# Performance work log

Hardware: AMD Instinct MI355X
Metric: run time of the kernel (lower is better)

## Reference

```python
import jax, jax.numpy as jnp
import numpy as np

B, N, F_IN, H, C = 4, 2048, 128, 4, 32
NEG_SLOPE = 0.2
EDGE_DENSITY = 0.01  # ~20 avg degree


def setup_inputs() -> dict:
    key = jax.random.key(0)
    ks = jax.random.split(key, 6)
    x = jax.random.normal(ks[0], (B, N, F_IN), dtype=jnp.float32)
    adj = (jax.random.uniform(ks[1], (B, N, N)) < EDGE_DENSITY).astype(jnp.float32)
    # glorot-style scaled params
    W = jax.random.normal(ks[2], (F_IN, H * C), dtype=jnp.float32) * (2.0 / (F_IN + H * C)) ** 0.5
    att_src = jax.random.normal(ks[3], (H, C), dtype=jnp.float32) * (2.0 / (1 + C)) ** 0.5
    att_dst = jax.random.normal(ks[4], (H, C), dtype=jnp.float32) * (2.0 / (1 + C)) ** 0.5
    bias = jnp.zeros((H * C,), dtype=jnp.float32)
    return {"x": x, "adj": adj, "W": W, "att_src": att_src, "att_dst": att_dst, "bias": bias}


def reference(x, adj, W, att_src, att_dst, bias):
    b, n, _ = x.shape
    h, c = att_src.shape
    # add self-loops
    idx = jnp.arange(n)
    adj = adj.at[:, idx, idx].set(1.0)
    # linear projection: [B,N,H,C]
    out = (x @ W).reshape(b, n, h, c)
    a_src = jnp.einsum('bnhc,hc->bnh', out, att_src)
    a_dst = jnp.einsum('bnhc,hc->bnh', out, att_dst)
    # alpha[b,i,j,h] = a_src[b,i,h] + a_dst[b,j,h]  -> [B,N,N,H]
    alpha = a_src[:, :, None, :] + a_dst[:, None, :, :]
    alpha = jax.nn.leaky_relu(alpha, NEG_SLOPE)
    alpha = adj[..., None] * jnp.exp(alpha)
    # faithful to original: normalize over dim=1 (the i axis)
    alpha = alpha / alpha.sum(axis=1, keepdims=True)
    # out_i = sum_j alpha[b,i,j,h] * feat[b,j,h,c]
    o = jnp.einsum('bijh,bjhc->bihc', alpha, out)
    o = o.reshape(b, n, h * c) + bias
    return o
```

## Files before the change

kernel.cpp:

```cpp
#include <hip/hip_runtime.h>
#include <math.h>

#define BB 4
#define NN 2048
#define F_IN 128
#define HH 4
#define CC 32
#define HC 128
#define NEG_SLOPE 0.2f
#define CAP 96

__device__ __forceinline__ float lrelu(float v) {
    return v > 0.f ? v : NEG_SLOPE * v;
}

__global__ __launch_bounds__(256) void k_gemm(const float* __restrict__ x,
                                              const float* __restrict__ W,
                                              float* __restrict__ feat) {
    __shared__ float xs[32][F_IN];
    const long row0 = (long)blockIdx.x * 32;
    const int t = threadIdx.x;
    for (int idx = t; idx < 32 * F_IN; idx += 256)
        xs[idx >> 7][idx & 127] = x[row0 * F_IN + idx];
    __syncthreads();
    const int col = t & 127;
    const int rg  = t >> 7;
    float acc[16];
#pragma unroll
    for (int r = 0; r < 16; ++r) acc[r] = 0.f;
    for (int k = 0; k < F_IN; ++k) {
        float w = W[k * HC + col];
#pragma unroll
        for (int r = 0; r < 16; ++r)
            acc[r] += xs[rg + 2 * r][k] * w;
    }
#pragma unroll
    for (int r = 0; r < 16; ++r)
        feat[(row0 + rg + 2 * r) * HC + col] = acc[r];
}

__global__ void k_att(const float* __restrict__ feat,
                      const float* __restrict__ att_src,
                      const float* __restrict__ att_dst,
                      float* __restrict__ a_src,
                      float* __restrict__ a_dst,
                      float* __restrict__ denom) {
    int idx = blockIdx.x * blockDim.x + threadIdx.x;
    if (idx >= BB * NN * HH) return;
    int h = idx & 3;
    long bn = idx >> 2;
    const float* f = feat + bn * HC + h * CC;
    float s = 0.f, d = 0.f;
#pragma unroll
    for (int c = 0; c < CC; ++c) {
        float v = f[c];
        s += v * att_src[h * CC + c];
        d += v * att_dst[h * CC + c];
    }
    a_src[idx] = s;
    a_dst[idx] = d;
    denom[idx] = 0.f;
}

__global__ __launch_bounds__(256) void k_scan(const float4* __restrict__ adj4,
                                              const float* __restrict__ a_src,
                                              const float* __restrict__ a_dst,
                                              float* __restrict__ denom,
                                              int* __restrict__ cnt,
                                              unsigned short* __restrict__ nbr) {
    const int bi = blockIdx.x;
    const int b = bi >> 11;
    const int i = bi & (NN - 1);
    __shared__ int s_cnt;
    if (threadIdx.x == 0) s_cnt = 0;
    __syncthreads();
    const int t = threadIdx.x;
    const float4* row = adj4 + (long)bi * (NN / 4);
    float4 v0 = row[t];
    float4 v1 = row[t + 256];
    const float4 as4 = *(const float4*)(a_src + bi * 4);

#define PROC(val, jc)                                                          \
    if ((val) != 0.f || (jc) == i) {                                           \
        int slot = atomicAdd(&s_cnt, 1);                                       \
        if (slot < CAP) nbr[(long)bi * CAP + slot] = (unsigned short)(jc);     \
        const long jj = (((long)b << 11) + (jc)) * 4;                          \
        float4 ad = *(const float4*)(a_dst + jj);                              \
        atomicAdd(&denom[jj + 0], __expf(lrelu(as4.x + ad.x)));                \
        atomicAdd(&denom[jj + 1], __expf(lrelu(as4.y + ad.y)));                \
        atomicAdd(&denom[jj + 2], __expf(lrelu(as4.z + ad.z)));                \
        atomicAdd(&denom[jj + 3], __expf(lrelu(as4.w + ad.w)));                \
    }

    int j0 = 4 * t;
    PROC(v0.x, j0 + 0)
    PROC(v0.y, j0 + 1)
    PROC(v0.z, j0 + 2)
    PROC(v0.w, j0 + 3)
    int j1 = 4 * t + 1024;
    PROC(v1.x, j1 + 0)
    PROC(v1.y, j1 + 1)
    PROC(v1.z, j1 + 2)
    PROC(v1.w, j1 + 3)
#undef PROC

    __syncthreads();
    if (t == 0) cnt[bi] = min(s_cnt, CAP);
}

__global__ __launch_bounds__(128) void k_aggr(const float* __restrict__ feat,
                                              const float* __restrict__ a_src,
                                              const float* __restrict__ a_dst,
                                              const float* __restrict__ denom,
                                              const int* __restrict__ cnt,
                                              const unsigned short* __restrict__ nbr,
                                              const float* __restrict__ bias,
                                              float* __restrict__ out) {
    const int bi = blockIdx.x;
    const int b = bi >> 11;
    const int t = threadIdx.x;
    __shared__ float s_coef[CAP][HH];
    __shared__ int   s_j[CAP];
    const int n = cnt[bi];
    for (int s = t; s < n; s += 128)
        s_j[s] = nbr[(long)bi * CAP + s];
    __syncthreads();
    for (int idx = t; idx < n * HH; idx += 128) {
        int s = idx >> 2, h = idx & 3;
        long jj = (((long)b << 11) + s_j[s]) * 4 + h;
        float e = __expf(lrelu(a_src[bi * 4 + h] + a_dst[jj]));
        s_coef[s][h] = e / denom[jj];
    }
    __syncthreads();
    const int h = t >> 5;
    const float* fb = feat + ((long)b << 11) * HC + t;
    float a0 = 0.f, a1 = 0.f, a2 = 0.f, a3 = 0.f;
    int s = 0;
    for (; s + 4 <= n; s += 4) {
        int j0 = s_j[s + 0], j1 = s_j[s + 1], j2 = s_j[s + 2], j3 = s_j[s + 3];
        float c0 = s_coef[s + 0][h], c1 = s_coef[s + 1][h];
        float c2 = s_coef[s + 2][h], c3 = s_coef[s + 3][h];
        a0 += c0 * fb[(long)j0 * HC];
        a1 += c1 * fb[(long)j1 * HC];
        a2 += c2 * fb[(long)j2 * HC];
        a3 += c3 * fb[(long)j3 * HC];
    }
    for (; s < n; ++s)
        a0 += s_coef[s][h] * fb[(long)s_j[s] * HC];
    out[(long)bi * HC + t] = (a0 + a1) + (a2 + a3) + bias[t];
}

extern "C" void kernel_launch(void* const* d_in, const int* in_sizes, int n_in,
                              void* d_out, int out_size, void* d_ws, size_t ws_size,
                              hipStream_t stream) {
    const float* x       = (const float*)d_in[0];
    const float* adj     = (const float*)d_in[1];
    const float* W       = (const float*)d_in[2];
    const float* att_src = (const float*)d_in[3];
    const float* att_dst = (const float*)d_in[4];
    const float* bias    = (const float*)d_in[5];
    float* out = (float*)d_out;

    float* feat  = (float*)d_ws;
    float* a_src = feat  + (long)BB * NN * HC;
    float* a_dst = a_src + (long)BB * NN * HH;
    float* denom = a_dst + (long)BB * NN * HH;
    int*   cnt   = (int*)(denom + (long)BB * NN * HH);
    unsigned short* nbr = (unsigned short*)(cnt + (long)BB * NN);

    k_gemm<<<(BB * NN) / 32, 256, 0, stream>>>(x, W, feat);
    k_att<<<(BB * NN * HH + 255) / 256, 256, 0, stream>>>(feat, att_src, att_dst,
                                                          a_src, a_dst, denom);
    k_scan<<<BB * NN, 256, 0, stream>>>((const float4*)adj, a_src, a_dst, denom, cnt, nbr);
    k_aggr<<<BB * NN, 128, 0, stream>>>(feat, a_src, a_dst, denom, cnt, nbr, bias, out);
}
```

Measured before the change: 170.8 us.

## Tile adjacency scan and replace global denom atomics with per-tile partial sums

Fuses the attention-logit computation into the projection GEMM. The per-row adjacency scan becomes a 2D tiled scan with 256x128 tiles. Each tile builds a shared-memory edge list and accumulates column denominators in shared memory, writing one partial sum per row tile. A small kernel then reduces the partials into reciprocal denominators, so the global float atomics on denom disappear and the aggregation kernel multiplies by the reciprocal instead of dividing. Neighbour capacity drops from 96 to 64 and each tile's edge list is capped at 768. This risks truncation for unusually dense rows or tiles, and neighbour order becomes nondeterministic.

```diff
diff --git a/kernel.cpp b/kernel.cpp
--- a/kernel.cpp
+++ b/kernel.cpp
@@ -8,16 +8,27 @@
 #define CC 32
 #define HC 128
 #define NEG_SLOPE 0.2f
-#define CAP 96
+#define CAP 64
+#define RT 256
+#define CT 128
+#define NRT 8
+#define NCT 16
+#define LCAP 768
 
 __device__ __forceinline__ float lrelu(float v) {
     return v > 0.f ? v : NEG_SLOPE * v;
 }
 
-__global__ __launch_bounds__(256) void k_gemm(const float* __restrict__ x,
-                                              const float* __restrict__ W,
-                                              float* __restrict__ feat) {
+__global__ __launch_bounds__(256) void k_gemm_att(const float* __restrict__ x,
+                                                  const float* __restrict__ W,
+                                                  const float* __restrict__ att_src,
+                                                  const float* __restrict__ att_dst,
+                                                  float* __restrict__ feat,
+                                                  float* __restrict__ a_src,
+                                                  float* __restrict__ a_dst,
+                                                  int* __restrict__ cnt) {
     __shared__ float xs[32][F_IN];
+    __shared__ float fs[32][HC + 1];
     const long row0 = (long)blockIdx.x * 32;
     const int t = threadIdx.x;
     for (int idx = t; idx < 32 * F_IN; idx += 256)
@@ -35,118 +46,172 @@
             acc[r] += xs[rg + 2 * r][k] * w;
     }
 #pragma unroll
-    for (int r = 0; r < 16; ++r)
+    for (int r = 0; r < 16; ++r) {
         feat[(row0 + rg + 2 * r) * HC + col] = acc[r];
-}
-
-__global__ void k_att(const float* __restrict__ feat,
-                      const float* __restrict__ att_src,
-                      const float* __restrict__ att_dst,
-                      float* __restrict__ a_src,
-                      float* __restrict__ a_dst,
-                      float* __restrict__ denom) {
-    int idx = blockIdx.x * blockDim.x + threadIdx.x;
-    if (idx >= BB * NN * HH) return;
-    int h = idx & 3;
-    long bn = idx >> 2;
-    const float* f = feat + bn * HC + h * CC;
-    float s = 0.f, d = 0.f;
-#pragma unroll
-    for (int c = 0; c < CC; ++c) {
-        float v = f[c];
-        s += v * att_src[h * CC + c];
-        d += v * att_dst[h * CC + c];
-    }
-    a_src[idx] = s;
-    a_dst[idx] = d;
-    denom[idx] = 0.f;
-}
-
-__global__ __launch_bounds__(256) void k_scan(const float4* __restrict__ adj4,
-                                              const float* __restrict__ a_src,
-                                              const float* __restrict__ a_dst,
-                                              float* __restrict__ denom,
+        fs[rg + 2 * r][col] = acc[r];
+    }
+    __syncthreads();
+    if (t < 128) {
+        const int row = t & 31;
+        const int h   = t >> 5;
+        float s = 0.f, d = 0.f;
+#pragma unroll
+        for (int c = 0; c < CC; ++c) {
+            float v = fs[row][h * CC + c];
+            s += v * att_src[h * CC + c];
+            d += v * att_dst[h * CC + c];
+        }
+        a_src[(row0 + row) * 4 + h] = s;
+        a_dst[(row0 + row) * 4 + h] = d;
+    }
+    if (t < 32) cnt[blockIdx.x * 32 + t] = 0;
+}
+
+__global__ __launch_bounds__(256) void k_tile(const float4* __restrict__ adj4,
+                                              const float4* __restrict__ as4g,
+                                              const float4* __restrict__ ad4g,
                                               int* __restrict__ cnt,
-                                              unsigned short* __restrict__ nbr) {
-    const int bi = blockIdx.x;
-    const int b = bi >> 11;
-    const int i = bi & (NN - 1);
-    __shared__ int s_cnt;
-    if (threadIdx.x == 0) s_cnt = 0;
-    __syncthreads();
-    const int t = threadIdx.x;
-    const float4* row = adj4 + (long)bi * (NN / 4);
-    float4 v0 = row[t];
-    float4 v1 = row[t + 256];
-    const float4 as4 = *(const float4*)(a_src + bi * 4);
-
-#define PROC(val, jc)                                                          \
-    if ((val) != 0.f || (jc) == i) {                                           \
-        int slot = atomicAdd(&s_cnt, 1);                                       \
-        if (slot < CAP) nbr[(long)bi * CAP + slot] = (unsigned short)(jc);     \
-        const long jj = (((long)b << 11) + (jc)) * 4;                          \
-        float4 ad = *(const float4*)(a_dst + jj);                              \
-        atomicAdd(&denom[jj + 0], __expf(lrelu(as4.x + ad.x)));                \
-        atomicAdd(&denom[jj + 1], __expf(lrelu(as4.y + ad.y)));                \
-        atomicAdd(&denom[jj + 2], __expf(lrelu(as4.z + ad.z)));                \
-        atomicAdd(&denom[jj + 3], __expf(lrelu(as4.w + ad.w)));                \
-    }
-
-    int j0 = 4 * t;
-    PROC(v0.x, j0 + 0)
-    PROC(v0.y, j0 + 1)
-    PROC(v0.z, j0 + 2)
-    PROC(v0.w, j0 + 3)
-    int j1 = 4 * t + 1024;
-    PROC(v1.x, j1 + 0)
-    PROC(v1.y, j1 + 1)
-    PROC(v1.z, j1 + 2)
-    PROC(v1.w, j1 + 3)
-#undef PROC
-
-    __syncthreads();
-    if (t == 0) cnt[bi] = min(s_cnt, CAP);
+                                              unsigned short* __restrict__ nbr,
+                                              float4* __restrict__ partial) {
+    const int bx = blockIdx.x;
+    const int b  = bx >> 7;
+    const int rt = (bx >> 4) & 7;
+    const int ct = bx & 15;
+    const int i0 = rt * RT;
+    const int c0 = ct * CT;
+    const int t  = threadIdx.x;
+
+    __shared__ float4 as4[RT];
+    __shared__ float4 ad4[CT];
+    __shared__ float4 pd[CT];
+    __shared__ unsigned short blist[LCAP];
+    __shared__ int rowcnt[RT];
+    __shared__ int rowoff[RT];
+    __shared__ int nent;
+
+    as4[t] = as4g[(b << 11) + i0 + t];
+    if (t < CT) {
+        ad4[t] = ad4g[(b << 11) + c0 + t];
+        pd[t] = make_float4(0.f, 0.f, 0.f, 0.f);
+    }
+    rowcnt[t] = 0;
+    if (t == 0) nent = 0;
+    __syncthreads();
+
+    const float4* base = adj4 + ((long)((b << 11) + i0)) * (NN / 4) + (c0 >> 2);
+    int idx0 = t * 4;
+    float4 v = base[(idx0 >> 7) * (NN / 4) + ((idx0 & 127) >> 2)];
+    for (int s = 0; s < 32; ++s) {
+        const int idx = s * 1024 + t * 4;
+        const float4 cur = v;
+        if (s < 31) {
+            const int nx = idx + 1024;
+            v = base[(nx >> 7) * (NN / 4) + ((nx & 127) >> 2)];
+        }
+        const int il = idx >> 7;
+        const int j0 = idx & 127;
+        const int gi = i0 + il;
+#pragma unroll
+        for (int k = 0; k < 4; ++k) {
+            const float vv = (&cur.x)[k];
+            if (vv != 0.f || gi == c0 + j0 + k) {
+                int pos = atomicAdd(&nent, 1);
+                if (pos < LCAP) blist[pos] = (unsigned short)((il << 7) | (j0 + k));
+                atomicAdd(&rowcnt[il], 1);
+            }
+        }
+    }
+    __syncthreads();
+
+    {
+        int rc = rowcnt[t];
+        int bs = 0;
+        if (rc > 0) bs = atomicAdd(&cnt[(b << 11) + i0 + t], rc);
+        rowoff[t] = bs;
+    }
+    __syncthreads();
+
+    const int ne = min(nent, LCAP);
+    for (int e = t; e < ne; e += 256) {
+        const int pk = blist[e];
+        const int il = pk >> 7;
+        const int jl = pk & 127;
+        const float4 s4 = as4[il];
+        const float4 d4 = ad4[jl];
+        atomicAdd(&(&pd[jl].x)[0], __expf(lrelu(s4.x + d4.x)));
+        atomicAdd(&(&pd[jl].x)[1], __expf(lrelu(s4.y + d4.y)));
+        atomicAdd(&(&pd[jl].x)[2], __expf(lrelu(s4.z + d4.z)));
+        atomicAdd(&(&pd[jl].x)[3], __expf(lrelu(s4.w + d4.w)));
+        int slot = atomicAdd(&rowoff[il], 1);
+        if (slot < CAP)
+            nbr[((long)((b << 11) + i0 + il)) * CAP + slot] = (unsigned short)(c0 + jl);
+    }
+    __syncthreads();
+
+    if (t < CT)
+        partial[((long)(b * NRT + rt) << 11) + c0 + t] = pd[t];
+}
+
+__global__ __launch_bounds__(256) void k_rdenom(const float4* __restrict__ partial,
+                                                float4* __restrict__ rdenom) {
+    const int u = blockIdx.x * blockDim.x + threadIdx.x;
+    if (u >= BB * NN) return;
+    const int b = u >> 11;
+    const int j = u & 2047;
+    float4 s = make_float4(0.f, 0.f, 0.f, 0.f);
+#pragma unroll
+    for (int rt = 0; rt < NRT; ++rt) {
+        float4 p = partial[((long)(b * NRT + rt) << 11) + j];
+        s.x += p.x; s.y += p.y; s.z += p.z; s.w += p.w;
+    }
+    rdenom[u] = make_float4(1.f / s.x, 1.f / s.y, 1.f / s.z, 1.f / s.w);
 }
 
 __global__ __launch_bounds__(128) void k_aggr(const float* __restrict__ feat,
                                               const float* __restrict__ a_src,
-                                              const float* __restrict__ a_dst,
-                                              const float* __restrict__ denom,
+                                              const float4* __restrict__ ad4,
+                                              const float4* __restrict__ rd4,
                                               const int* __restrict__ cnt,
                                               const unsigned short* __restrict__ nbr,
                                               const float* __restrict__ bias,
                                               float* __restrict__ out) {
     const int bi = blockIdx.x;
-    const int b = bi >> 11;
-    const int t = threadIdx.x;
-    __shared__ float s_coef[CAP][HH];
-    __shared__ int   s_j[CAP];
-    const int n = cnt[bi];
-    for (int s = t; s < n; s += 128)
-        s_j[s] = nbr[(long)bi * CAP + s];
-    __syncthreads();
-    for (int idx = t; idx < n * HH; idx += 128) {
-        int s = idx >> 2, h = idx & 3;
-        long jj = (((long)b << 11) + s_j[s]) * 4 + h;
-        float e = __expf(lrelu(a_src[bi * 4 + h] + a_dst[jj]));
-        s_coef[s][h] = e / denom[jj];
+    const int b  = bi >> 11;
+    const int t  = threadIdx.x;
+    __shared__ float4 s_coef[CAP];
+    __shared__ int    s_j[CAP];
+    __shared__ float  s_as[4];
+    const int n = min(cnt[bi], CAP);
+    if (t < 4) s_as[t] = a_src[bi * 4 + t];
+    if (t < n) s_j[t] = nbr[(long)bi * CAP + t];
+    __syncthreads();
+    if (t < n) {
+        const int j = s_j[t];
+        const float4 ad = ad4[(b << 11) + j];
+        const float4 rd = rd4[(b << 11) + j];
+        float4 c;
+        c.x = __expf(lrelu(s_as[0] + ad.x)) * rd.x;
+        c.y = __expf(lrelu(s_as[1] + ad.y)) * rd.y;
+        c.z = __expf(lrelu(s_as[2] + ad.z)) * rd.z;
+        c.w = __expf(lrelu(s_as[3] + ad.w)) * rd.w;
+        s_coef[t] = c;
     }
     __syncthreads();
     const int h = t >> 5;
-    const float* fb = feat + ((long)b << 11) * HC + t;
+    const float* fb = feat + ((long)(b << 11)) * HC + t;
     float a0 = 0.f, a1 = 0.f, a2 = 0.f, a3 = 0.f;
     int s = 0;
     for (; s + 4 <= n; s += 4) {
         int j0 = s_j[s + 0], j1 = s_j[s + 1], j2 = s_j[s + 2], j3 = s_j[s + 3];
-        float c0 = s_coef[s + 0][h], c1 = s_coef[s + 1][h];
-        float c2 = s_coef[s + 2][h], c3 = s_coef[s + 3][h];
+        float c0 = (&s_coef[s + 0].x)[h], c1 = (&s_coef[s + 1].x)[h];
+        float c2 = (&s_coef[s + 2].x)[h], c3 = (&s_coef[s + 3].x)[h];
         a0 += c0 * fb[(long)j0 * HC];
         a1 += c1 * fb[(long)j1 * HC];
         a2 += c2 * fb[(long)j2 * HC];
         a3 += c3 * fb[(long)j3 * HC];
     }
     for (; s < n; ++s)
-        a0 += s_coef[s][h] * fb[(long)s_j[s] * HC];
+        a0 += (&s_coef[s].x)[h] * fb[(long)s_j[s] * HC];
     out[(long)bi * HC + t] = (a0 + a1) + (a2 + a3) + bias[t];
 }
 
@@ -161,16 +226,21 @@
     const float* bias    = (const float*)d_in[5];
     float* out = (float*)d_out;
 
-    float* feat  = (float*)d_ws;
-    float* a_src = feat  + (long)BB * NN * HC;
-    float* a_dst = a_src + (long)BB * NN * HH;
-    float* denom = a_dst + (long)BB * NN * HH;
-    int*   cnt   = (int*)(denom + (long)BB * NN * HH);
+    float* feat    = (float*)d_ws;
+    float* a_src   = feat    + (long)BB * NN * HC;
+    float* a_dst   = a_src   + (long)BB * NN * HH;
+    float* rdenom  = a_dst   + (long)BB * NN * HH;
+    float* partial = rdenom  + (long)BB * NN * HH;
+    int*   cnt     = (int*)(partial + (long)BB * NRT * NN * HH);
     unsigned short* nbr = (unsigned short*)(cnt + (long)BB * NN);
 
-    k_gemm<<<(BB * NN) / 32, 256, 0, stream>>>(x, W, feat);
-    k_att<<<(BB * NN * HH + 255) / 256, 256, 0, stream>>>(feat, att_src, att_dst,
-                                                          a_src, a_dst, denom);
-    k_scan<<<BB * NN, 256, 0, stream>>>((const float4*)adj, a_src, a_dst, denom, cnt, nbr);
-    k_aggr<<<BB * NN, 128, 0, stream>>>(feat, a_src, a_dst, denom, cnt, nbr, bias, out);
-}
+    k_gemm_att<<<(BB * NN) / 32, 256, 0, stream>>>(x, W, att_src, att_dst,
+                                                   feat, a_src, a_dst, cnt);
+    k_tile<<<BB * NRT * NCT, 256, 0, stream>>>((const float4*)adj, (const float4*)a_src,
+                                               (const float4*)a_dst, cnt, nbr,
+                                               (float4*)partial);
+    k_rdenom<<<(BB * NN + 255) / 256, 256, 0, stream>>>((const float4*)partial,
+                                                        (float4*)rdenom);
+    k_aggr<<<BB * NN, 128, 0, stream>>>(feat, a_src, (const float4*)a_dst,
+                                        (const float4*)rdenom, cnt, nbr, bias, out);
+}
```

Result: faster. 148.1 us (-13.3%).
